# Kernel tuning notes

Measured on AMD Instinct MI355X. Metric: run time of the kernel, lower is better.

The kernel has to match this reference:

```python
import jax, jax.numpy as jnp
import numpy as np
from jax import lax

B, T, D, U = 128, 1024, 256, 48


def setup_inputs() -> dict:
    key = jax.random.key(0)
    k1, k2, k3 = jax.random.split(key, 3)
    x = jax.random.normal(k1, (B, T, D), dtype=jnp.float32)
    kernel = jax.random.normal(k2, (D, U), dtype=jnp.float32) * (1.0 / np.sqrt(D))
    bias = jnp.zeros((U,), dtype=jnp.float32)
    chain_kernel = jax.random.normal(k3, (U, U), dtype=jnp.float32)
    return {"x": x, "kernel": kernel, "bias": bias, "chain_kernel": chain_kernel}


def _viterbi_decode(logits, trans):
    # logits: [B, T, U], trans: [U, U]; full-length sequences (mask=None)
    init_state = logits[:, 0]  # [B, U]
    steps = jnp.swapaxes(logits[:, 1:], 0, 1)  # [T-1, B, U]

    def fwd(state, logit_t):
        # scores[b, i, j] = state[b, i] + trans[i, j]
        scores = state[:, :, None] + trans[None]  # [B, U, U]
        bp = jnp.argmax(scores, axis=1)            # [B, U] best prev tag
        new_state = logit_t + jnp.max(scores, axis=1)
        return new_state, bp

    final_state, bps = lax.scan(fwd, init_state, steps)  # bps: [T-1, B, U]
    last_tag = jnp.argmax(final_state, axis=-1)          # [B]

    def back(tag, bp):
        prev = jnp.take_along_axis(bp, tag[:, None], axis=1)[:, 0]
        return prev, prev

    # reverse scan emits tags for t = 0..T-2 in forward time order
    _, tags_head = lax.scan(back, last_tag, bps, reverse=True)  # [T-1, B]
    tags = jnp.concatenate([tags_head, last_tag[None]], axis=0)  # [T, B]
    return jnp.transpose(tags)  # [B, T]


def reference(x, kernel, bias, chain_kernel):
    # _dense_layer: linear activation -> x @ kernel + bias
    logits = jnp.einsum('btd,du->btu', x, kernel) + bias  # [B, T, U]
    pred_ids = _viterbi_decode(logits, chain_kernel)       # [B, T] int
    return pred_ids.astype(jnp.float32)
```

## Files before the change

### kernel.cpp

```cpp
#include <hip/hip_runtime.h>
#include <cstdint>

#define B_ 128
#define T_ 1024
#define D_ 256
#define U_ 48

__global__ __launch_bounds__(256, 1) void k_logits(const float* __restrict__ x,
                                                   const float* __restrict__ kern,
                                                   const float* __restrict__ bias,
                                                   float* __restrict__ logits) {
    __shared__ float K[D_ * U_];
    __shared__ float bsh[U_];
    const int tid = threadIdx.x;
    for (int i = tid; i < D_ * U_; i += 256) K[i] = kern[i];
    if (tid < U_) bsh[tid] = bias[tid];
    __syncthreads();

    const long row0 = (long)blockIdx.x * 256 + tid;
    const long row1 = row0 + (long)B_ * T_ / 2;
    const float4* xr0 = (const float4*)(x + row0 * D_);
    const float4* xr1 = (const float4*)(x + row1 * D_);

    float a0[U_], a1[U_];
#pragma unroll
    for (int u = 0; u < U_; ++u) { a0[u] = 0.0f; a1[u] = 0.0f; }

#pragma unroll 1
    for (int blk = 0; blk < D_ / 32; ++blk) {
        float4 xa[8], xb[8];
#pragma unroll
        for (int i = 0; i < 8; ++i) xa[i] = xr0[blk * 8 + i];
#pragma unroll
        for (int i = 0; i < 8; ++i) xb[i] = xr1[blk * 8 + i];

#pragma unroll
        for (int i = 0; i < 8; ++i) {
            const int d4 = blk * 8 + i;
            const float xc0[4] = {xa[i].x, xa[i].y, xa[i].z, xa[i].w};
            const float xc1[4] = {xb[i].x, xb[i].y, xb[i].z, xb[i].w};
#pragma unroll
            for (int c = 0; c < 4; ++c) {
                const float4* kp = (const float4*)&K[(d4 * 4 + c) * U_];
                const float s0 = xc0[c], s1 = xc1[c];
#pragma unroll
                for (int u4 = 0; u4 < U_ / 4; ++u4) {
                    float4 kv = kp[u4];
                    a0[u4*4+0] += s0 * kv.x;  a1[u4*4+0] += s1 * kv.x;
                    a0[u4*4+1] += s0 * kv.y;  a1[u4*4+1] += s1 * kv.y;
                    a0[u4*4+2] += s0 * kv.z;  a1[u4*4+2] += s1 * kv.z;
                    a0[u4*4+3] += s0 * kv.w;  a1[u4*4+3] += s1 * kv.w;
                }
            }
        }
    }

    float4* o0 = (float4*)(logits + row0 * U_);
    float4* o1 = (float4*)(logits + row1 * U_);
#pragma unroll
    for (int i = 0; i < U_ / 4; ++i) {
        float4 v0, v1;
        v0.x = a0[i*4+0] + bsh[i*4+0];  v1.x = a1[i*4+0] + bsh[i*4+0];
        v0.y = a0[i*4+1] + bsh[i*4+1];  v1.y = a1[i*4+1] + bsh[i*4+1];
        v0.z = a0[i*4+2] + bsh[i*4+2];  v1.z = a1[i*4+2] + bsh[i*4+2];
        v0.w = a0[i*4+3] + bsh[i*4+3];  v1.w = a1[i*4+3] + bsh[i*4+3];
        o0[i] = v0;
        o1[i] = v1;
    }
}

__device__ __forceinline__ float step_max_lds(const float4* sb, const float2* tc2) {
    float n0 = -3.0e38f, n1 = -3.0e38f, n2 = -3.0e38f, n3 = -3.0e38f;
#pragma unroll
    for (int k = 0; k < U_ / 4; k += 4) {
        float4 s0 = sb[k + 0];
        float4 s1 = sb[k + 1];
        float4 s2 = sb[k + 2];
        float4 s3 = sb[k + 3];
        float2 p0 = make_float2(s0.x + tc2[2*k+0].x, s0.y + tc2[2*k+0].y);
        float2 p1 = make_float2(s0.z + tc2[2*k+1].x, s0.w + tc2[2*k+1].y);
        float2 p2 = make_float2(s1.x + tc2[2*k+2].x, s1.y + tc2[2*k+2].y);
        float2 p3 = make_float2(s1.z + tc2[2*k+3].x, s1.w + tc2[2*k+3].y);
        float2 p4 = make_float2(s2.x + tc2[2*k+4].x, s2.y + tc2[2*k+4].y);
        float2 p5 = make_float2(s2.z + tc2[2*k+5].x, s2.w + tc2[2*k+5].y);
        float2 p6 = make_float2(s3.x + tc2[2*k+6].x, s3.y + tc2[2*k+6].y);
        float2 p7 = make_float2(s3.z + tc2[2*k+7].x, s3.w + tc2[2*k+7].y);
        n0 = fmaxf(n0, fmaxf(fmaxf(p0.x, p0.y), fmaxf(p1.x, p1.y)));
        n1 = fmaxf(n1, fmaxf(fmaxf(p2.x, p2.y), fmaxf(p3.x, p3.y)));
        n2 = fmaxf(n2, fmaxf(fmaxf(p4.x, p4.y), fmaxf(p5.x, p5.y)));
        n3 = fmaxf(n3, fmaxf(fmaxf(p6.x, p6.y), fmaxf(p7.x, p7.y)));
    }
    return fmaxf(fmaxf(n0, n1), fmaxf(n2, n3));
}

__global__ __launch_bounds__(64, 1) void k_forward(const float* __restrict__ trans,
                                                   const float* __restrict__ logits,
                                                   float* __restrict__ delta) {
    __shared__ float4 sbuf[2][U_ / 4];
    const int lane = threadIdx.x;
    const int b = blockIdx.x;
    const int u = (lane < U_) ? lane : (U_ - 1);

    float2 tc2[U_ / 2];
#pragma unroll
    for (int v = 0; v < U_; v += 2) {
        tc2[v / 2].x = trans[v * U_ + u];
        tc2[v / 2].y = trans[(v + 1) * U_ + u];
    }

    const float* lin = logits + (long)b * T_ * U_;
    float* dout = delta + (long)b * T_ * U_;

    float state = lin[u];
    dout[u] = state;
    ((float*)sbuf[0])[u] = state;

    float pf[8];
#pragma unroll
    for (int i = 0; i < 8; ++i) pf[i] = lin[(1 + i) * U_ + u];

    const float* lp = lin + 9 * U_ + u;
    float* dp = dout + 1 * U_ + u;

#pragma unroll 1
    for (int g = 0; g < 127; ++g) {
#pragma unroll
        for (int j = 0; j < 8; ++j) {
            const float logit = pf[j];
            pf[j] = lp[j * U_];

            const float4* sb = sbuf[j & 1];
            const float m = step_max_lds(sb, tc2);
            state = logit + m;
            ((float*)sbuf[(j & 1) ^ 1])[u] = state;
            dp[j * U_] = state;
        }
        lp += 8 * U_;
        dp += 8 * U_;
    }

#pragma unroll
    for (int j = 0; j < 7; ++j) {
        const float logit = pf[j];
        const float4* sb = sbuf[j & 1];
        const float m = step_max_lds(sb, tc2);
        state = logit + m;
        ((float*)sbuf[(j & 1) ^ 1])[u] = state;
        dp[j * U_] = state;
    }
}

__global__ __launch_bounds__(64, 1) void k_forward_inplace(const float* __restrict__ trans,
                                                           float* __restrict__ delta) {
    __shared__ float4 sbuf[2][U_ / 4];
    const int lane = threadIdx.x;
    const int b = blockIdx.x;
    const int u = (lane < U_) ? lane : (U_ - 1);

    float2 tc2[U_ / 2];
#pragma unroll
    for (int v = 0; v < U_; v += 2) {
        tc2[v / 2].x = trans[v * U_ + u];
        tc2[v / 2].y = trans[(v + 1) * U_ + u];
    }

    float* base = delta + (long)b * T_ * U_;
    float state = base[u];
    ((float*)sbuf[0])[u] = state;

#pragma unroll 1
    for (int t = 1; t < T_; ++t) {
        const float logit = base[(long)t * U_ + u];
        const float m = step_max_lds(sbuf[(t - 1) & 1], tc2);
        state = logit + m;
        ((float*)sbuf[t & 1])[u] = state;
        base[(long)t * U_ + u] = state;
    }
}

#define BP_ROWS 32
__global__ __launch_bounds__(64, 1) void k_bp(const float* __restrict__ trans,
                                              const float* __restrict__ delta,
                                              unsigned char* __restrict__ bp) {
    __shared__ float sbuf[2][U_];
    const int lane = threadIdx.x;
    const int u = (lane < U_) ? lane : (U_ - 1);

    float tc[U_];
#pragma unroll
    for (int v = 0; v < U_; ++v) tc[v] = trans[v * U_ + u];

    const int NROW = B_ * (T_ - 1);
    const int row0 = blockIdx.x * BP_ROWS;
    if (row0 >= NROW) return;

    int b = row0 / (T_ - 1);
    int tm1 = row0 - b * (T_ - 1);

    float dval = delta[((long)b * T_ + tm1) * U_ + u];

#pragma unroll 1
    for (int i = 0; i < BP_ROWS; ++i) {
        const int row = row0 + i;
        if (row >= NROW) break;

        sbuf[i & 1][u] = dval;

        int bn = b, tn = tm1 + 1;
        if (tn == T_ - 1) { tn = 0; bn = b + 1; }
        float dnext = 0.0f;
        if (row + 1 < NROW) dnext = delta[((long)bn * T_ + tn) * U_ + u];

        const float4* sb4 = (const float4*)sbuf[i & 1];
        float best = -3.4e38f;
        int bi = 0;
#pragma unroll
        for (int k = 0; k < U_ / 4; ++k) {
            float4 s = sb4[k];
            float c0 = s.x + tc[4*k+0];
            float c1 = s.y + tc[4*k+1];
            float c2 = s.z + tc[4*k+2];
            float c3 = s.w + tc[4*k+3];
            bi = (c0 > best) ? 4*k+0 : bi;  best = fmaxf(best, c0);
            bi = (c1 > best) ? 4*k+1 : bi;  best = fmaxf(best, c1);
            bi = (c2 > best) ? 4*k+2 : bi;  best = fmaxf(best, c2);
            bi = (c3 > best) ? 4*k+3 : bi;  best = fmaxf(best, c3);
        }
        bp[(long)row * U_ + u] = (unsigned char)bi;

        b = bn; tm1 = tn; dval = dnext;
    }
}

__global__ __launch_bounds__(64) void k_back(const float* __restrict__ delta,
                                             const unsigned char* __restrict__ bp,
                                             float* __restrict__ out) {
    __shared__ unsigned char bpl[(T_ - 1) * U_];
    __shared__ float tags[T_];
    __shared__ float fin[U_];
    const int lane = threadIdx.x;
    const int b = blockIdx.x;

    const uint32_t* src = (const uint32_t*)(bp + (long)b * (T_ - 1) * U_);
    uint32_t* dst = (uint32_t*)bpl;
    const int NW = (T_ - 1) * U_ / 4;
    for (int i = lane; i < NW; i += 64) dst[i] = src[i];
    if (lane < U_) fin[lane] = delta[((long)b * T_ + (T_ - 1)) * U_ + lane];
    __syncthreads();

    if (lane == 0) {
        float best = fin[0];
        int tag = 0;
        for (int uu = 1; uu < U_; ++uu)
            if (fin[uu] > best) { best = fin[uu]; tag = uu; }
        tags[T_ - 1] = (float)tag;
        for (int t = T_ - 1; t >= 1; --t) {
            tag = bpl[(t - 1) * U_ + tag];
            tags[t - 1] = (float)tag;
        }
    }
    __syncthreads();

    float* o = out + (long)b * T_;
    for (int i = lane; i < T_; i += 64) o[i] = tags[i];
}

extern "C" void kernel_launch(void* const* d_in, const int* in_sizes, int n_in,
                              void* d_out, int out_size, void* d_ws, size_t ws_size,
                              hipStream_t stream) {
    const float* x     = (const float*)d_in[0];
    const float* kern  = (const float*)d_in[1];
    const float* bias  = (const float*)d_in[2];
    const float* trans = (const float*)d_in[3];
    float* out = (float*)d_out;

    const size_t NBT = (size_t)B_ * T_ * U_ * sizeof(float);

    float* logits = (float*)d_ws;
    const bool two_buf = ws_size >= 2 * NBT + (size_t)B_ * T_ * U_;
    float* delta = two_buf ? (float*)((char*)d_ws + NBT) : logits;
    unsigned char* bp = (unsigned char*)d_ws + (two_buf ? 2 * NBT : NBT);

    const int NROW = B_ * (T_ - 1);
    const int bp_grid = (NROW + BP_ROWS - 1) / BP_ROWS;

    k_logits<<<(B_ * T_ / 2) / 256, 256, 0, stream>>>(x, kern, bias, logits);
    if (two_buf)
        k_forward<<<B_, 64, 0, stream>>>(trans, logits, delta);
    else
        k_forward_inplace<<<B_, 64, 0, stream>>>(trans, logits);
    k_bp  <<<bp_grid, 64, 0, stream>>>(trans, delta, bp);
    k_back<<<B_,      64, 0, stream>>>(delta, bp, out);
}
```

Baseline: 515.7 us.

## Register-tile logits GEMM 8x8 per thread and parallelize Viterbi backtrace via map composition

The logits kernel now gives each thread an 8-row by 8-unit register tile (192 threads, 512 blocks), so kernel values from shared memory are reused across 8 rows and x values across 8 outputs, instead of each thread computing two full 48-wide rows. The backtrace kernel splits the 1023 steps into 64 segments of 16: each lane composes its segment's backpointer maps for all 48 start tags, one lane chains the 64 composed maps, and then every lane replays its own segment in parallel. This replaces a 1023-step serial dependent LDS chain with two 16-step parallel phases and one 64-step serial phase. The cost is extra LDS traffic and registers (48-entry cur arrays), and strided x row loads in the GEMM.

```diff
diff --git a/kernel.cpp b/kernel.cpp
--- a/kernel.cpp
+++ b/kernel.cpp
@@ -6,66 +6,72 @@
 #define D_ 256
 #define U_ 48
 
-__global__ __launch_bounds__(256, 1) void k_logits(const float* __restrict__ x,
+__global__ __launch_bounds__(192, 1) void k_logits(const float* __restrict__ x,
                                                    const float* __restrict__ kern,
                                                    const float* __restrict__ bias,
                                                    float* __restrict__ logits) {
     __shared__ float K[D_ * U_];
     __shared__ float bsh[U_];
     const int tid = threadIdx.x;
-    for (int i = tid; i < D_ * U_; i += 256) K[i] = kern[i];
+    for (int i = tid; i < D_ * U_; i += 192) K[i] = kern[i];
     if (tid < U_) bsh[tid] = bias[tid];
     __syncthreads();
 
-    const long row0 = (long)blockIdx.x * 256 + tid;
-    const long row1 = row0 + (long)B_ * T_ / 2;
-    const float4* xr0 = (const float4*)(x + row0 * D_);
-    const float4* xr1 = (const float4*)(x + row1 * D_);
-
-    float a0[U_], a1[U_];
-#pragma unroll
-    for (int u = 0; u < U_; ++u) { a0[u] = 0.0f; a1[u] = 0.0f; }
-
-#pragma unroll 1
-    for (int blk = 0; blk < D_ / 32; ++blk) {
-        float4 xa[8], xb[8];
-#pragma unroll
-        for (int i = 0; i < 8; ++i) xa[i] = xr0[blk * 8 + i];
-#pragma unroll
-        for (int i = 0; i < 8; ++i) xb[i] = xr1[blk * 8 + i];
-
-#pragma unroll
-        for (int i = 0; i < 8; ++i) {
-            const int d4 = blk * 8 + i;
-            const float xc0[4] = {xa[i].x, xa[i].y, xa[i].z, xa[i].w};
-            const float xc1[4] = {xb[i].x, xb[i].y, xb[i].z, xb[i].w};
-#pragma unroll
-            for (int c = 0; c < 4; ++c) {
-                const float4* kp = (const float4*)&K[(d4 * 4 + c) * U_];
-                const float s0 = xc0[c], s1 = xc1[c];
-#pragma unroll
-                for (int u4 = 0; u4 < U_ / 4; ++u4) {
-                    float4 kv = kp[u4];
-                    a0[u4*4+0] += s0 * kv.x;  a1[u4*4+0] += s1 * kv.x;
-                    a0[u4*4+1] += s0 * kv.y;  a1[u4*4+1] += s1 * kv.y;
-                    a0[u4*4+2] += s0 * kv.z;  a1[u4*4+2] += s1 * kv.z;
-                    a0[u4*4+3] += s0 * kv.w;  a1[u4*4+3] += s1 * kv.w;
-                }
+    const int rg = tid & 31;
+    const int us = tid >> 5;
+    const int u0 = us * 8;
+    const long row0 = (long)blockIdx.x * 256 + (long)rg * 8;
+    const float* xbase = x + row0 * D_;
+
+    float acc[8][8];
+#pragma unroll
+    for (int r = 0; r < 8; ++r)
+#pragma unroll
+        for (int j = 0; j < 8; ++j) acc[r][j] = 0.0f;
+
+#pragma unroll 1
+    for (int c = 0; c < D_ / 8; ++c) {
+        float4 k0[8], k1[8];
+#pragma unroll
+        for (int dd = 0; dd < 8; ++dd) {
+            const float4* kp = (const float4*)&K[(c * 8 + dd) * U_ + u0];
+            k0[dd] = kp[0];
+            k1[dd] = kp[1];
+        }
+#pragma unroll
+        for (int r = 0; r < 8; ++r) {
+            const float4* xp = (const float4*)(xbase + (long)r * D_ + c * 8);
+            const float4 xa = xp[0];
+            const float4 xb = xp[1];
+            const float xs[8] = {xa.x, xa.y, xa.z, xa.w, xb.x, xb.y, xb.z, xb.w};
+#pragma unroll
+            for (int dd = 0; dd < 8; ++dd) {
+                acc[r][0] += xs[dd] * k0[dd].x;
+                acc[r][1] += xs[dd] * k0[dd].y;
+                acc[r][2] += xs[dd] * k0[dd].z;
+                acc[r][3] += xs[dd] * k0[dd].w;
+                acc[r][4] += xs[dd] * k1[dd].x;
+                acc[r][5] += xs[dd] * k1[dd].y;
+                acc[r][6] += xs[dd] * k1[dd].z;
+                acc[r][7] += xs[dd] * k1[dd].w;
             }
         }
     }
 
-    float4* o0 = (float4*)(logits + row0 * U_);
-    float4* o1 = (float4*)(logits + row1 * U_);
-#pragma unroll
-    for (int i = 0; i < U_ / 4; ++i) {
+#pragma unroll
+    for (int r = 0; r < 8; ++r) {
         float4 v0, v1;
-        v0.x = a0[i*4+0] + bsh[i*4+0];  v1.x = a1[i*4+0] + bsh[i*4+0];
-        v0.y = a0[i*4+1] + bsh[i*4+1];  v1.y = a1[i*4+1] + bsh[i*4+1];
-        v0.z = a0[i*4+2] + bsh[i*4+2];  v1.z = a1[i*4+2] + bsh[i*4+2];
-        v0.w = a0[i*4+3] + bsh[i*4+3];  v1.w = a1[i*4+3] + bsh[i*4+3];
-        o0[i] = v0;
-        o1[i] = v1;
+        v0.x = acc[r][0] + bsh[u0 + 0];
+        v0.y = acc[r][1] + bsh[u0 + 1];
+        v0.z = acc[r][2] + bsh[u0 + 2];
+        v0.w = acc[r][3] + bsh[u0 + 3];
+        v1.x = acc[r][4] + bsh[u0 + 4];
+        v1.y = acc[r][5] + bsh[u0 + 5];
+        v1.z = acc[r][6] + bsh[u0 + 6];
+        v1.w = acc[r][7] + bsh[u0 + 7];
+        float4* op = (float4*)(logits + (row0 + r) * U_ + u0);
+        op[0] = v0;
+        op[1] = v1;
     }
 }
 
@@ -232,20 +238,37 @@
     }
 }
 
-__global__ __launch_bounds__(64) void k_back(const float* __restrict__ delta,
-                                             const unsigned char* __restrict__ bp,
-                                             float* __restrict__ out) {
-    __shared__ unsigned char bpl[(T_ - 1) * U_];
+__global__ __launch_bounds__(64, 1) void k_back(const float* __restrict__ delta,
+                                                const unsigned char* __restrict__ bp,
+                                                float* __restrict__ out) {
+    __shared__ unsigned char bpl[T_ * U_];
+    __shared__ unsigned char maps[64][U_];
     __shared__ float tags[T_];
     __shared__ float fin[U_];
+    __shared__ unsigned char bt[65];
     const int lane = threadIdx.x;
     const int b = blockIdx.x;
 
-    const uint32_t* src = (const uint32_t*)(bp + (long)b * (T_ - 1) * U_);
-    uint32_t* dst = (uint32_t*)bpl;
-    const int NW = (T_ - 1) * U_ / 4;
-    for (int i = lane; i < NW; i += 64) dst[i] = src[i];
+    const uint4* src = (const uint4*)(bp + (long)b * (T_ - 1) * U_);
+    uint4* dst = (uint4*)bpl;
+#pragma unroll 1
+    for (int i = lane; i < (T_ - 1) * U_ / 16; i += 64) dst[i] = src[i];
+    if (lane < U_) bpl[(T_ - 1) * U_ + lane] = (unsigned char)lane;
     if (lane < U_) fin[lane] = delta[((long)b * T_ + (T_ - 1)) * U_ + lane];
+    __syncthreads();
+
+    int cur[U_];
+#pragma unroll
+    for (int e = 0; e < U_; ++e) cur[e] = e;
+    const int klo = lane * 16;
+#pragma unroll 1
+    for (int s = 15; s >= 0; --s) {
+        const unsigned char* rowp = &bpl[(klo + s) * U_];
+#pragma unroll
+        for (int e = 0; e < U_; ++e) cur[e] = rowp[cur[e]];
+    }
+#pragma unroll
+    for (int e = 0; e < U_; ++e) maps[lane][e] = (unsigned char)cur[e];
     __syncthreads();
 
     if (lane == 0) {
@@ -253,11 +276,19 @@
         int tag = 0;
         for (int uu = 1; uu < U_; ++uu)
             if (fin[uu] > best) { best = fin[uu]; tag = uu; }
-        tags[T_ - 1] = (float)tag;
-        for (int t = T_ - 1; t >= 1; --t) {
-            tag = bpl[(t - 1) * U_ + tag];
-            tags[t - 1] = (float)tag;
-        }
+        bt[64] = (unsigned char)tag;
+        for (int i = 63; i >= 0; --i) {
+            tag = maps[i][tag];
+            bt[i] = (unsigned char)tag;
+        }
+    }
+    __syncthreads();
+
+    int e = bt[lane + 1];
+#pragma unroll 1
+    for (int s = 15; s >= 0; --s) {
+        e = bpl[(klo + s) * U_ + e];
+        tags[klo + s] = (float)e;
     }
     __syncthreads();
 
@@ -284,7 +315,7 @@
     const int NROW = B_ * (T_ - 1);
     const int bp_grid = (NROW + BP_ROWS - 1) / BP_ROWS;
 
-    k_logits<<<(B_ * T_ / 2) / 256, 256, 0, stream>>>(x, kern, bias, logits);
+    k_logits<<<512, 192, 0, stream>>>(x, kern, bias, logits);
     if (two_buf)
         k_forward<<<B_, 64, 0, stream>>>(trans, logits, delta);
     else
```

Result: slower. 559.6 us (+8.5%).
